# Optimization experiments

Hardware: AMD Instinct MI355X
Metric: run time of the kernel (lower is better)

## Reference

```python
import jax, jax.numpy as jnp
import numpy as np

N = 50000      # nodes
E = 800000     # edges (avg degree 16)
LM = 768       # lm_input_dim
H = 192        # hidden_dim = 32*6
B6 = 32        # per-branch dim = hidden_dim/6
SLOPE = 0.01   # nn.LeakyReLU default negative slope


def setup_inputs() -> dict:
    key = jax.random.key(0)
    ks = jax.random.split(key, 32)
    f = lambda i, shape, s=0.05: (jax.random.normal(ks[i], shape, jnp.float32) * s)
    inp = {
        "pre_x": f(0, (N, LM)),
        "x": f(1, (N, LM)),
        "edge_index": jax.random.randint(ks[2], (2, E), 0, N),
        "edge_type": jax.random.randint(ks[3], (E,), 0, 3),
        "num_prop": f(4, (N, 5)),
        "num_category": f(5, (N, 1)),
        "des_tensor": f(6, (N, LM)),
        "tweet_tensor": f(7, (N, LM)),
        # parameters (torch nn.Linear convention: W is [out, in], y = x @ W.T + b)
        "W_des": f(8, (B6, LM)), "b_des": f(9, (B6,)),
        "W_tweet": f(10, (B6, LM)), "b_tweet": f(11, (B6,)),
        "W_tweet_tr": f(12, (B6, LM)), "b_tweet_tr": f(13, (B6,)),
        "W_prop": f(14, (B6, 5)), "b_prop": f(15, (B6,)),
        "W_cat": f(16, (B6, 1)), "b_cat": f(17, (B6,)),
        "W_text": f(18, (B6, LM)), "b_text": f(19, (B6,)),
        "W_in": f(20, (H, H)), "b_in": f(21, (H,)),
        "W_c1": f(22, (H, H)), "b_c1": f(23, (H,)),
        "W_c2": f(24, (H, H)), "b_c2": f(25, (H,)),
        "W_o1": f(26, (96, H)), "b_o1": f(27, (96,)),
        "W_o2": f(28, (2, 96)), "b_o2": f(29, (2,)),
    }
    return inp


def _gcn_conv(h, W, b, src, dst):
    """PyG GCNConv: symmetric-normalized aggregation with added self-loops.
    out[v] = sum_{u->v} (d_u d_v)^{-1/2} (h_u W^T) + (1/d_v) (h_v W^T) + b
    where d includes the self-loop (+1)."""
    n = h.shape[0]
    hW = h @ W.T                                                  # [N, H]
    deg = jax.ops.segment_sum(jnp.ones(src.shape[0], h.dtype), dst,
                              num_segments=n) + 1.0               # [N]
    dinv = jax.lax.rsqrt(deg)
    norm = dinv[src] * dinv[dst]                                  # [E]
    agg = jax.ops.segment_sum(hW[src] * norm[:, None], dst,
                              num_segments=n)                     # [N, H]
    return agg + hW * (1.0 / deg)[:, None] + b


def reference(pre_x, x, edge_index, edge_type, num_prop, num_category,
              des_tensor, tweet_tensor,
              W_des, b_des, W_tweet, b_tweet, W_tweet_tr, b_tweet_tr,
              W_prop, b_prop, W_cat, b_cat, W_text, b_text,
              W_in, b_in, W_c1, b_c1, W_c2, b_c2,
              W_o1, b_o1, W_o2, b_o2):
    lrelu = lambda v: jax.nn.leaky_relu(v, SLOPE)
    branch = lambda t, W, b: lrelu(t @ W.T + b)   # dropout is identity in eval

    d = branch(des_tensor, W_des, b_des)
    pre_t = branch(pre_x, W_tweet, b_tweet)
    t = branch(x, W_tweet_tr, b_tweet_tr)
    n = branch(num_prop, W_prop, b_prop)
    c = branch(num_category, W_cat, b_cat)
    tw = branch(tweet_tensor, W_text, b_text)

    h = jnp.concatenate((n, c, d, tw, pre_t, t), axis=1)          # [N, 192]
    h = lrelu(h @ W_in.T + b_in)

    src, dst = edge_index[0], edge_index[1]
    h = _gcn_conv(h, W_c1, b_c1, src, dst)
    h = _gcn_conv(h, W_c2, b_c2, src, dst)

    em = lrelu(h @ W_o1.T + b_o1)                                 # [N, 96]
    out = em @ W_o2.T + b_o2                                      # [N, 2]
    return (out, em)
```

## Files before the change

kernel.cpp:

```cpp
#include <hip/hip_runtime.h>

#define NN 50000
#define EE 800000
#define LMD 768
#define HD 192
#define SLOPE 0.01f

typedef short bf16x8 __attribute__((ext_vector_type(8)));
typedef float f32x4 __attribute__((ext_vector_type(4)));
typedef unsigned short u16;

__device__ __forceinline__ float lrelu(float v){ return v > 0.f ? v : SLOPE * v; }

__device__ __forceinline__ u16 f2bf(float f){
    unsigned u = __float_as_uint(f);
    u += 0x7FFF + ((u >> 16) & 1u);
    return (u16)(u >> 16);
}
__device__ __forceinline__ float bf2f(u16 v){
    return __uint_as_float(((unsigned)v) << 16);
}
__device__ __forceinline__ bf16x8 as_bf8(float4 v){
    union { float4 f; bf16x8 b; } u; u.f = v; return u.b;
}

__global__ __launch_bounds__(256) void k_prep(
    const float* __restrict__ W0, const float* __restrict__ W1,
    const float* __restrict__ W2, const float* __restrict__ W3,
    const float* __restrict__ Win, const float* __restrict__ Wc1,
    const float* __restrict__ Wc2, const float* __restrict__ Wo1,
    u16* __restrict__ out)
{
    int m = blockIdx.y;
    int idx = blockIdx.x * 256 + threadIdx.x;
    const float* src; int nelem; int K;
    switch (m) {
      case 0: src = W0;  nelem = 32*768;  K = 768; break;
      case 1: src = W1;  nelem = 32*768;  K = 768; break;
      case 2: src = W2;  nelem = 32*768;  K = 768; break;
      case 3: src = W3;  nelem = 32*768;  K = 768; break;
      case 4: src = Win; nelem = 192*192; K = 192; break;
      case 5: src = Wc1; nelem = 192*192; K = 192; break;
      case 6: src = Wc2; nelem = 192*192; K = 192; break;
      default: src = Wo1; nelem = 96*192; K = 192; break;
    }
    if (idx >= nelem) return;
    u16 v = f2bf(src[idx]);
    int c = idx / K, k = idx - c * K;
    int cb = c >> 4, lr = c & 15;
    int sg = k >> 5, kk = k & 31, hi = kk >> 3, j = kk & 7;
    int lane = hi * 16 + lr;
    size_t dst;
    if (m < 4)      dst = (size_t)m * 24576 + (sg * 2 + cb) * 512 + lane * 8 + j;
    else if (m < 7) dst = 98304 + (size_t)(m - 4) * 36864 + (sg * 12 + cb) * 512 + lane * 8 + j;
    else            dst = 208896 + (size_t)(sg * 6 + cb) * 512 + lane * 8 + j;
    out[dst] = v;
}

#define BR_LOAD(R0, R1, c) { \
  _Pragma("unroll") for (int rt = 0; rt < 4; ++rt) { \
    const float* p_ = abase[rt] + (c) * 128; \
    R0[rt] = *(const float4*)p_; R1[rt] = *(const float4*)(p_ + 4); } \
  _Pragma("unroll") for (int rt = 0; rt < 4; ++rt) { \
    asm volatile("" :: "v"(R0[rt].x), "v"(R0[rt].y), "v"(R0[rt].z), "v"(R0[rt].w)); \
    asm volatile("" :: "v"(R1[rt].x), "v"(R1[rt].y), "v"(R1[rt].z), "v"(R1[rt].w)); } }

#define BR_WRITE(R0, R1) { \
  _Pragma("unroll") for (int rt = 0; rt < 4; ++rt) { \
    uint4 pk_; \
    pk_.x = (unsigned)f2bf(R0[rt].x) | ((unsigned)f2bf(R0[rt].y) << 16); \
    pk_.y = (unsigned)f2bf(R0[rt].z) | ((unsigned)f2bf(R0[rt].w) << 16); \
    pk_.z = (unsigned)f2bf(R1[rt].x) | ((unsigned)f2bf(R1[rt].y) << 16); \
    pk_.w = (unsigned)f2bf(R1[rt].z) | ((unsigned)f2bf(R1[rt].w) << 16); \
    *(uint4*)(Asg + wrIdx[rt]) = pk_; } }

#define BR_COMPUTE(fb) { \
  _Pragma("unroll") for (int sgl = 0; sgl < 4; ++sgl) { \
    bf16x8 af_ = *(const bf16x8*)(Asg + wbase + sgl * 512 + rdOff); \
    _Pragma("unroll") for (int cb = 0; cb < 2; ++cb) { \
      bf16x8 bf_ = *(const bf16x8*)(Bs + (fb) + (sgl * 2 + cb) * 512 + l * 8); \
      acc[cb] = __builtin_amdgcn_mfma_f32_16x16x32_bf16(af_, bf_, acc[cb], 0, 0, 0); } } }

#define BR_STAGEB(half) { \
  const uint4* s_ = (const uint4*)(Wb + (half) * 12288); uint4* d_ = (uint4*)Bs; \
  _Pragma("unroll") for (int i = 0; i < 6; ++i) d_[i * 256 + t] = s_[i * 256 + t]; }

__global__ __launch_bounds__(256) void k_branch(
    const float* __restrict__ des, const float* __restrict__ twt,
    const float* __restrict__ prex, const float* __restrict__ xx,
    const u16* __restrict__ Wf,
    const float* __restrict__ bd, const float* __restrict__ btx,
    const float* __restrict__ btw, const float* __restrict__ btr,
    u16* __restrict__ h)
{
    __shared__ u16 Bs[12288];
    __shared__ u16 Asg[8192];
    const int br = blockIdx.y;
    const float* A; const float* bias; int colBase;
    switch (br) {
      case 0:  A = des;  bias = bd;  colBase = 64;  break;
      case 1:  A = twt;  bias = btx; colBase = 96;  break;
      case 2:  A = prex; bias = btw; colBase = 128; break;
      default: A = xx;   bias = btr; colBase = 160; break;
    }
    const u16* Wb = Wf + br * 24576;

    const int t = threadIdx.x, w = t >> 6, l = t & 63;
    const int hi = l >> 4, lr = l & 15;
    const int rowBase = blockIdx.x * 64;
    const int wbase = w * 2048;
    const int rdOff = (l ^ hi) * 8;

    const float* abase[4];
    int wrIdx[4];
    #pragma unroll
    for (int rt = 0; rt < 4; ++rt) {
        int r = rowBase + w * 16 + rt * 4 + hi;
        if (r >= NN) r = NN - 1;
        abase[rt] = A + (size_t)r * LMD + lr * 8;
        int slot = ((l & 3) << 4) | (rt * 4 + hi);
        wrIdx[rt] = wbase + (lr >> 2) * 512 + (slot ^ (l & 3)) * 8;
    }

    f32x4 acc[2] = {};
    float4 a0[4], a1[4], b0[4], b1[4];

    BR_LOAD(a0, a1, 0);
    BR_STAGEB(0);
    __syncthreads();
    BR_LOAD(b0, b1, 1);
    BR_WRITE(a0, a1);  BR_COMPUTE(0);
    BR_LOAD(a0, a1, 2);
    BR_WRITE(b0, b1);  BR_COMPUTE(4096);
    BR_LOAD(b0, b1, 3);
    BR_WRITE(a0, a1);  BR_COMPUTE(8192);
    __syncthreads();
    BR_STAGEB(1);
    __syncthreads();
    BR_LOAD(a0, a1, 4);
    BR_WRITE(b0, b1);  BR_COMPUTE(0);
    BR_LOAD(b0, b1, 5);
    BR_WRITE(a0, a1);  BR_COMPUTE(4096);
    BR_WRITE(b0, b1);  BR_COMPUTE(8192);

    #pragma unroll
    for (int cb = 0; cb < 2; ++cb) {
        int cl = cb * 16 + lr;
        float bv = bias[cl];
        #pragma unroll
        for (int rg = 0; rg < 4; ++rg) {
            int r = rowBase + w * 16 + hi * 4 + rg;
            if (r < NN)
                h[(size_t)r * HD + colBase + cl] = f2bf(lrelu(acc[cb][rg] + bv));
        }
    }
}

template<bool BIAS, bool LRELU>
__global__ __launch_bounds__(512) void k_hgemm(
    const u16* __restrict__ A, const u16* __restrict__ Wf,
    const float* __restrict__ bias, u16* __restrict__ out)
{
    __shared__ u16 Bs[36864];
    const int t = threadIdx.x, w = t >> 6, l = t & 63;
    const int hi = l >> 4, lr = l & 15;
    const int rowBase = blockIdx.x * 128;
    {
        const uint4* s_ = (const uint4*)Wf; uint4* d_ = (uint4*)Bs;
        #pragma unroll
        for (int i = 0; i < 9; ++i) d_[i * 512 + t] = s_[i * 512 + t];
    }
    int r0 = rowBase + w * 16 + lr;
    int rowc = r0 < NN ? r0 : NN - 1;
    const u16* ap = A + (size_t)rowc * HD;
    float4 araw[6];
    #pragma unroll
    for (int sg = 0; sg < 6; ++sg) {
        araw[sg] = *(const float4*)(ap + sg * 32 + hi * 8);
        asm volatile("" :: "v"(araw[sg].x), "v"(araw[sg].y), "v"(araw[sg].z), "v"(araw[sg].w));
    }
    __syncthreads();

    f32x4 acc[12] = {};
    #pragma unroll
    for (int sg = 0; sg < 6; ++sg) {
        bf16x8 af = as_bf8(araw[sg]);
        #pragma unroll
        for (int cb = 0; cb < 12; ++cb) {
            bf16x8 bf = *(const bf16x8*)(Bs + (sg * 12 + cb) * 512 + l * 8);
            acc[cb] = __builtin_amdgcn_mfma_f32_16x16x32_bf16(af, bf, acc[cb], 0, 0, 0);
        }
    }

    #pragma unroll
    for (int cb = 0; cb < 12; ++cb) {
        int cl = cb * 16 + lr;
        float bv = BIAS ? bias[cl] : 0.f;
        #pragma unroll
        for (int rg = 0; rg < 4; ++rg) {
            int r = rowBase + w * 16 + hi * 4 + rg;
            if (r < NN) {
                float v = acc[cb][rg] + bv;
                if (LRELU) v = lrelu(v);
                out[(size_t)r * HD + cl] = f2bf(v);
            }
        }
    }
}

__global__ __launch_bounds__(512) void k_final(
    const u16* __restrict__ A, const u16* __restrict__ Wf,
    const float* __restrict__ b1, const float* __restrict__ W2,
    const float* __restrict__ b2, float* __restrict__ em, float* __restrict__ out)
{
    __shared__ u16 Bs[18432];
    const int t = threadIdx.x, w = t >> 6, l = t & 63;
    const int hi = l >> 4, lr = l & 15;
    const int rowBase = blockIdx.x * 128;
    {
        const uint4* s_ = (const uint4*)Wf; uint4* d_ = (uint4*)Bs;
        #pragma unroll
        for (int i = 0; i < 5; ++i) { int idx = i * 512 + t; if (idx < 2304) d_[idx] = s_[idx]; }
    }
    int r0 = rowBase + w * 16 + lr;
    int rowc = r0 < NN ? r0 : NN - 1;
    const u16* ap = A + (size_t)rowc * HD;
    float4 araw[6];
    #pragma unroll
    for (int sg = 0; sg < 6; ++sg) {
        araw[sg] = *(const float4*)(ap + sg * 32 + hi * 8);
        asm volatile("" :: "v"(araw[sg].x), "v"(araw[sg].y), "v"(araw[sg].z), "v"(araw[sg].w));
    }
    __syncthreads();

    f32x4 acc[6] = {};
    #pragma unroll
    for (int sg = 0; sg < 6; ++sg) {
        bf16x8 af = as_bf8(araw[sg]);
        #pragma unroll
        for (int cb = 0; cb < 6; ++cb) {
            bf16x8 bf = *(const bf16x8*)(Bs + (sg * 6 + cb) * 512 + l * 8);
            acc[cb] = __builtin_amdgcn_mfma_f32_16x16x32_bf16(af, bf, acc[cb], 0, 0, 0);
        }
    }

    float w2v[2][6], bv[6];
    #pragma unroll
    for (int cb = 0; cb < 6; ++cb) {
        bv[cb] = b1[cb * 16 + lr];
        w2v[0][cb] = W2[cb * 16 + lr];
        w2v[1][cb] = W2[96 + cb * 16 + lr];
    }

    #pragma unroll
    for (int rg = 0; rg < 4; ++rg) {
        int r = rowBase + w * 16 + hi * 4 + rg;
        float o0 = 0.f, o1 = 0.f;
        #pragma unroll
        for (int cb = 0; cb < 6; ++cb) {
            float v = lrelu(acc[cb][rg] + bv[cb]);
            if (r < NN) em[(size_t)r * 96 + cb * 16 + lr] = v;
            o0 += v * w2v[0][cb];
            o1 += v * w2v[1][cb];
        }
        #pragma unroll
        for (int d = 1; d < 16; d <<= 1) {
            o0 += __shfl_xor(o0, d);
            o1 += __shfl_xor(o1, d);
        }
        if (lr == 0 && r < NN) {
            out[r * 2 + 0] = o0 + b2[0];
            out[r * 2 + 1] = o1 + b2[1];
        }
    }
}

__global__ __launch_bounds__(256) void k_small_branch(
    const float* __restrict__ nprop, const float* __restrict__ ncat,
    const float* __restrict__ Wp, const float* __restrict__ bp,
    const float* __restrict__ Wc, const float* __restrict__ bc,
    u16* __restrict__ h)
{
    int idx = blockIdx.x * 256 + threadIdx.x;
    if (idx >= NN * 64) return;
    int row = idx >> 6, c = idx & 63;
    float acc;
    if (c < 32) {
        acc = bp[c];
        #pragma unroll
        for (int k = 0; k < 5; ++k) acc += nprop[row * 5 + k] * Wp[c * 5 + k];
    } else {
        int cc = c - 32;
        acc = bc[cc] + ncat[row] * Wc[cc];
    }
    h[(size_t)row * HD + c] = f2bf(lrelu(acc));
}

__global__ void k_count(const int* __restrict__ ei, int* __restrict__ deg)
{
    int e = blockIdx.x * 256 + threadIdx.x;
    if (e < EE) atomicAdd(&deg[ei[EE + e]], 1);
}

__global__ void k_deginv(const int* __restrict__ deg, float* __restrict__ dinv, float* __restrict__ invdeg)
{
    int v = blockIdx.x * 256 + threadIdx.x;
    if (v < NN) {
        float d = (float)(deg[v] + 1);
        dinv[v] = rsqrtf(d);
        invdeg[v] = 1.0f / d;
    }
}

__global__ __launch_bounds__(1024) void k_scan1(const int* __restrict__ deg, int* __restrict__ rp, int* __restrict__ part)
{
    __shared__ int sh[1024];
    int tid = threadIdx.x, i = blockIdx.x * 1024 + tid;
    int x = (i < NN) ? deg[i] : 0;
    sh[tid] = x;
    __syncthreads();
    for (int off = 1; off < 1024; off <<= 1) {
        int y = (tid >= off) ? sh[tid - off] : 0;
        __syncthreads();
        sh[tid] += y;
        __syncthreads();
    }
    if (i < NN) rp[i] = sh[tid] - x;
    if (tid == 1023) part[blockIdx.x] = sh[tid];
}

__global__ void k_scan2(int* part, int nb, int* rp)
{
    if (threadIdx.x == 0 && blockIdx.x == 0) {
        int run = 0;
        for (int b = 0; b < nb; ++b) { int t = part[b]; part[b] = run; run += t; }
        rp[NN] = run;
    }
}

__global__ void k_scan3(int* rp, const int* __restrict__ part)
{
    int i = blockIdx.x * 256 + threadIdx.x;
    if (i < NN) rp[i] += part[i >> 10];
}

__global__ void k_fill(const int* __restrict__ ei, const float* __restrict__ dinv,
                       int* __restrict__ cursor, int* __restrict__ cs, float* __restrict__ nrm)
{
    int e = blockIdx.x * 256 + threadIdx.x;
    if (e >= EE) return;
    int s = ei[e], d = ei[EE + e];
    int pos = atomicAdd(&cursor[d], 1);
    cs[pos] = s;
    nrm[pos] = dinv[s] * dinv[d];
}

__global__ __launch_bounds__(240) void k_agg(const u16* __restrict__ hW,
    const int* __restrict__ rp, const int* __restrict__ cs, const float* __restrict__ nrm,
    const float* __restrict__ invdeg, const float* __restrict__ bias, u16* __restrict__ out)
{
    int v = blockIdx.x * 5 + threadIdx.y;
    int f0 = threadIdx.x * 4;
    int s0 = rp[v], s1 = rp[v + 1];
    float4 bv = *reinterpret_cast<const float4*>(bias + f0);
    ushort4 hv = *reinterpret_cast<const ushort4*>(hW + (size_t)v * HD + f0);
    float idg = invdeg[v];
    float a0 = bf2f(hv.x) * idg + bv.x;
    float a1 = bf2f(hv.y) * idg + bv.y;
    float a2 = bf2f(hv.z) * idg + bv.z;
    float a3 = bf2f(hv.w) * idg + bv.w;
    int i = s0;
    for (; i + 4 <= s1; i += 4) {
        int c0 = cs[i], c1 = cs[i+1], c2 = cs[i+2], c3 = cs[i+3];
        float n0 = nrm[i], n1 = nrm[i+1], n2 = nrm[i+2], n3 = nrm[i+3];
        ushort4 g0 = *reinterpret_cast<const ushort4*>(hW + (size_t)c0 * HD + f0);
        ushort4 g1 = *reinterpret_cast<const ushort4*>(hW + (size_t)c1 * HD + f0);
        ushort4 g2 = *reinterpret_cast<const ushort4*>(hW + (size_t)c2 * HD + f0);
        ushort4 g3 = *reinterpret_cast<const ushort4*>(hW + (size_t)c3 * HD + f0);
        a0 += bf2f(g0.x) * n0; a1 += bf2f(g0.y) * n0; a2 += bf2f(g0.z) * n0; a3 += bf2f(g0.w) * n0;
        a0 += bf2f(g1.x) * n1; a1 += bf2f(g1.y) * n1; a2 += bf2f(g1.z) * n1; a3 += bf2f(g1.w) * n1;
        a0 += bf2f(g2.x) * n2; a1 += bf2f(g2.y) * n2; a2 += bf2f(g2.z) * n2; a3 += bf2f(g2.w) * n2;
        a0 += bf2f(g3.x) * n3; a1 += bf2f(g3.y) * n3; a2 += bf2f(g3.z) * n3; a3 += bf2f(g3.w) * n3;
    }
    for (; i < s1; ++i) {
        int c = cs[i]; float n = nrm[i];
        ushort4 g = *reinterpret_cast<const ushort4*>(hW + (size_t)c * HD + f0);
        a0 += bf2f(g.x) * n; a1 += bf2f(g.y) * n; a2 += bf2f(g.z) * n; a3 += bf2f(g.w) * n;
    }
    ushort4 o;
    o.x = f2bf(a0); o.y = f2bf(a1); o.z = f2bf(a2); o.w = f2bf(a3);
    *reinterpret_cast<ushort4*>(out + (size_t)v * HD + f0) = o;
}

extern "C" void kernel_launch(void* const* d_in, const int* in_sizes, int n_in,
                              void* d_out, int out_size, void* d_ws, size_t ws_size,
                              hipStream_t stream)
{
    const float* pre_x = (const float*)d_in[0];
    const float* x     = (const float*)d_in[1];
    const int*   ei    = (const int*)d_in[2];
    const float* nprop = (const float*)d_in[4];
    const float* ncat  = (const float*)d_in[5];
    const float* des   = (const float*)d_in[6];
    const float* twt   = (const float*)d_in[7];
    const float* W_des  = (const float*)d_in[8],  *b_des  = (const float*)d_in[9];
    const float* W_tw   = (const float*)d_in[10], *b_tw   = (const float*)d_in[11];
    const float* W_tr   = (const float*)d_in[12], *b_tr   = (const float*)d_in[13];
    const float* W_prop = (const float*)d_in[14], *b_prop = (const float*)d_in[15];
    const float* W_cat  = (const float*)d_in[16], *b_cat  = (const float*)d_in[17];
    const float* W_text = (const float*)d_in[18], *b_text = (const float*)d_in[19];
    const float* W_in   = (const float*)d_in[20], *b_in   = (const float*)d_in[21];
    const float* W_c1   = (const float*)d_in[22], *b_c1   = (const float*)d_in[23];
    const float* W_c2   = (const float*)d_in[24], *b_c2   = (const float*)d_in[25];
    const float* W_o1   = (const float*)d_in[26], *b_o1   = (const float*)d_in[27];
    const float* W_o2   = (const float*)d_in[28], *b_o2   = (const float*)d_in[29];

    char* base = (char*)d_ws;
    size_t off = 0;
    auto alloc = [&](size_t bytes) -> char* {
        char* p = base + off;
        off = (off + bytes + 255) & ~(size_t)255;
        return p;
    };
    u16*   hA     = (u16*)alloc((size_t)NN * HD * 2);
    u16*   hB     = (u16*)alloc((size_t)NN * HD * 2);
    u16*   hC     = (u16*)alloc((size_t)NN * HD * 2);
    u16*   Wprep  = (u16*)alloc((size_t)227328 * 2);
    float* dinv   = (float*)alloc((size_t)NN * 4);
    float* invdeg = (float*)alloc((size_t)NN * 4);
    int*   deg    = (int*)alloc((size_t)NN * 4);
    int*   rp     = (int*)alloc((size_t)(NN + 1) * 4);
    int*   cursor = (int*)alloc((size_t)NN * 4);
    int*   part   = (int*)alloc(64 * 4);
    int*   cs     = (int*)alloc((size_t)EE * 4);
    float* nrm    = (float*)alloc((size_t)EE * 4);
    (void)ws_size; (void)in_sizes; (void)n_in; (void)out_size;

    float* outp = (float*)d_out;
    float* em   = outp + (size_t)NN * 2;

    const int rb     = (NN + 255) / 256;
    const int rb64   = (NN + 63) / 64;
    const int rb128  = (NN + 127) / 128;
    const int eb     = (EE + 255) / 256;
    const int nb1024 = (NN + 1023) / 1024;

    hipMemsetAsync(deg, 0, (size_t)NN * 4, stream);
    hipLaunchKernelGGL(k_prep, dim3(144, 8), dim3(256), 0, stream,
        W_des, W_text, W_tw, W_tr, W_in, W_c1, W_c2, W_o1, Wprep);
    hipLaunchKernelGGL(k_count,  dim3(eb), dim3(256), 0, stream, ei, deg);
    hipLaunchKernelGGL(k_deginv, dim3(rb), dim3(256), 0, stream, deg, dinv, invdeg);
    hipLaunchKernelGGL(k_scan1,  dim3(nb1024), dim3(1024), 0, stream, deg, rp, part);
    hipLaunchKernelGGL(k_scan2,  dim3(1), dim3(1), 0, stream, part, nb1024, rp);
    hipLaunchKernelGGL(k_scan3,  dim3(rb), dim3(256), 0, stream, rp, part);
    hipMemcpyAsync(cursor, rp, (size_t)NN * 4, hipMemcpyDeviceToDevice, stream);
    hipLaunchKernelGGL(k_fill,   dim3(eb), dim3(256), 0, stream, ei, dinv, cursor, cs, nrm);

    hipLaunchKernelGGL(k_branch, dim3(rb64, 4), dim3(256), 0, stream,
        des, twt, pre_x, x, Wprep, b_des, b_text, b_tw, b_tr, hA);
    hipLaunchKernelGGL(k_small_branch, dim3((NN * 64 + 255) / 256), dim3(256), 0, stream,
        nprop, ncat, W_prop, b_prop, W_cat, b_cat, hA);

    hipLaunchKernelGGL((k_hgemm<true, true>),   dim3(rb128), dim3(512), 0, stream,
        hA, Wprep + 98304, b_in, hB);
    hipLaunchKernelGGL((k_hgemm<false, false>), dim3(rb128), dim3(512), 0, stream,
        hB, Wprep + 98304 + 36864, nullptr, hC);
    hipLaunchKernelGGL(k_agg, dim3(NN / 5), dim3(48, 5), 0, stream, hC, rp, cs, nrm, invdeg, b_c1, hA);
    hipLaunchKernelGGL((k_hgemm<false, false>), dim3(rb128), dim3(512), 0, stream,
        hA, Wprep + 98304 + 2 * 36864, nullptr, hB);
    hipLaunchKernelGGL(k_agg, dim3(NN / 5), dim3(48, 5), 0, stream, hB, rp, cs, nrm, invdeg, b_c2, hC);

    hipLaunchKernelGGL(k_final, dim3(rb128), dim3(512), 0, stream,
        hC, Wprep + 208896, b_o1, W_o2, b_o2, em, outp);
}
```

Before: 410.2 us.

## Stream branch activations via direct global-to-LDS loads with triple buffering

Rewrites the branch GEMM kernel to stage fp32 activation tiles straight into LDS using global_load_lds in a three-deep ring, with explicit vmcnt waits. The whole 32x768 weight slice now sits in LDS up front instead of being staged in two halves. This removes the register round-trip and the bf16 pack/write step for A, plus two block barriers. In exchange, bf16 conversion now happens after each LDS read, LDS use grows, and there are no barriers between waves (each wave reads only its own rows, which is fine).

```diff
diff --git a/kernel.cpp b/kernel.cpp
--- a/kernel.cpp
+++ b/kernel.cpp
@@ -23,6 +23,10 @@
 __device__ __forceinline__ bf16x8 as_bf8(float4 v){
     union { float4 f; bf16x8 b; } u; u.f = v; return u.b;
 }
+
+#define GLOAD16(gp, lp) __builtin_amdgcn_global_load_lds( \
+    (const __attribute__((address_space(1))) void*)(gp), \
+    (__attribute__((address_space(3))) void*)(lp), 16, 0, 0)
 
 __global__ __launch_bounds__(256) void k_prep(
     const float* __restrict__ W0, const float* __restrict__ W1,
@@ -57,34 +61,6 @@
     out[dst] = v;
 }
 
-#define BR_LOAD(R0, R1, c) { \
-  _Pragma("unroll") for (int rt = 0; rt < 4; ++rt) { \
-    const float* p_ = abase[rt] + (c) * 128; \
-    R0[rt] = *(const float4*)p_; R1[rt] = *(const float4*)(p_ + 4); } \
-  _Pragma("unroll") for (int rt = 0; rt < 4; ++rt) { \
-    asm volatile("" :: "v"(R0[rt].x), "v"(R0[rt].y), "v"(R0[rt].z), "v"(R0[rt].w)); \
-    asm volatile("" :: "v"(R1[rt].x), "v"(R1[rt].y), "v"(R1[rt].z), "v"(R1[rt].w)); } }
-
-#define BR_WRITE(R0, R1) { \
-  _Pragma("unroll") for (int rt = 0; rt < 4; ++rt) { \
-    uint4 pk_; \
-    pk_.x = (unsigned)f2bf(R0[rt].x) | ((unsigned)f2bf(R0[rt].y) << 16); \
-    pk_.y = (unsigned)f2bf(R0[rt].z) | ((unsigned)f2bf(R0[rt].w) << 16); \
-    pk_.z = (unsigned)f2bf(R1[rt].x) | ((unsigned)f2bf(R1[rt].y) << 16); \
-    pk_.w = (unsigned)f2bf(R1[rt].z) | ((unsigned)f2bf(R1[rt].w) << 16); \
-    *(uint4*)(Asg + wrIdx[rt]) = pk_; } }
-
-#define BR_COMPUTE(fb) { \
-  _Pragma("unroll") for (int sgl = 0; sgl < 4; ++sgl) { \
-    bf16x8 af_ = *(const bf16x8*)(Asg + wbase + sgl * 512 + rdOff); \
-    _Pragma("unroll") for (int cb = 0; cb < 2; ++cb) { \
-      bf16x8 bf_ = *(const bf16x8*)(Bs + (fb) + (sgl * 2 + cb) * 512 + l * 8); \
-      acc[cb] = __builtin_amdgcn_mfma_f32_16x16x32_bf16(af_, bf_, acc[cb], 0, 0, 0); } } }
-
-#define BR_STAGEB(half) { \
-  const uint4* s_ = (const uint4*)(Wb + (half) * 12288); uint4* d_ = (uint4*)Bs; \
-  _Pragma("unroll") for (int i = 0; i < 6; ++i) d_[i * 256 + t] = s_[i * 256 + t]; }
-
 __global__ __launch_bounds__(256) void k_branch(
     const float* __restrict__ des, const float* __restrict__ twt,
     const float* __restrict__ prex, const float* __restrict__ xx,
@@ -93,8 +69,9 @@
     const float* __restrict__ btw, const float* __restrict__ btr,
     u16* __restrict__ h)
 {
-    __shared__ u16 Bs[12288];
-    __shared__ u16 Asg[8192];
+    __shared__ u16 Ws_[24576];
+    __shared__ float Ab[3][64][32];
+
     const int br = blockIdx.y;
     const float* A; const float* bias; int colBase;
     switch (br) {
@@ -103,45 +80,60 @@
       case 2:  A = prex; bias = btw; colBase = 128; break;
       default: A = xx;   bias = btr; colBase = 160; break;
     }
-    const u16* Wb = Wf + br * 24576;
 
     const int t = threadIdx.x, w = t >> 6, l = t & 63;
     const int hi = l >> 4, lr = l & 15;
     const int rowBase = blockIdx.x * 64;
-    const int wbase = w * 2048;
-    const int rdOff = (l ^ hi) * 8;
-
-    const float* abase[4];
-    int wrIdx[4];
-    #pragma unroll
-    for (int rt = 0; rt < 4; ++rt) {
-        int r = rowBase + w * 16 + rt * 4 + hi;
-        if (r >= NN) r = NN - 1;
-        abase[rt] = A + (size_t)r * LMD + lr * 8;
-        int slot = ((l & 3) << 4) | (rt * 4 + hi);
-        wrIdx[rt] = wbase + (lr >> 2) * 512 + (slot ^ (l & 3)) * 8;
-    }
+
+    {
+        const uint4* s_ = (const uint4*)(Wf + br * 24576);
+        uint4* d_ = (uint4*)Ws_;
+        #pragma unroll
+        for (int i = 0; i < 12; ++i) d_[i * 256 + t] = s_[i * 256 + t];
+    }
+    __syncthreads();
+
+    const int rl_ = w * 16 + (l >> 3);
+    const int s16 = l & 7, g_ = s16 >> 1, hf = s16 & 1;
+
+#define STAGE(cc, bufi) { \
+    _Pragma("unroll") for (int i_ = 0; i_ < 2; ++i_) { \
+        int rl = rl_ + i_ * 8; \
+        int rg = rowBase + rl; if (rg >= NN) rg = NN - 1; \
+        const float* gp = A + (size_t)rg * LMD + (cc) * 32 + ((g_ ^ (rl & 3)) * 8 + hf * 4); \
+        GLOAD16(gp, &Ab[bufi][w * 16 + i_ * 8][0]); } }
+
+    STAGE(0, 0);
+    STAGE(1, 1);
 
     f32x4 acc[2] = {};
-    float4 a0[4], a1[4], b0[4], b1[4];
-
-    BR_LOAD(a0, a1, 0);
-    BR_STAGEB(0);
-    __syncthreads();
-    BR_LOAD(b0, b1, 1);
-    BR_WRITE(a0, a1);  BR_COMPUTE(0);
-    BR_LOAD(a0, a1, 2);
-    BR_WRITE(b0, b1);  BR_COMPUTE(4096);
-    BR_LOAD(b0, b1, 3);
-    BR_WRITE(a0, a1);  BR_COMPUTE(8192);
-    __syncthreads();
-    BR_STAGEB(1);
-    __syncthreads();
-    BR_LOAD(a0, a1, 4);
-    BR_WRITE(b0, b1);  BR_COMPUTE(0);
-    BR_LOAD(b0, b1, 5);
-    BR_WRITE(a0, a1);  BR_COMPUTE(4096);
-    BR_WRITE(b0, b1);  BR_COMPUTE(8192);
+
+    #pragma unroll
+    for (int c = 0; c < 24; ++c) {
+        if (c + 2 < 24) {
+            const int bufi = (c + 2) % 3;
+            STAGE(c + 2, bufi);
+        }
+        if (c < 22)      { asm volatile("s_waitcnt vmcnt(4)" ::: "memory"); }
+        else if (c == 22){ asm volatile("s_waitcnt vmcnt(2)" ::: "memory"); }
+        else             { asm volatile("s_waitcnt vmcnt(0)" ::: "memory"); }
+        __builtin_amdgcn_sched_barrier(0);
+
+        const float* ab = &Ab[c % 3][w * 16 + lr][(hi ^ (lr & 3)) * 8];
+        float4 lo = *(const float4*)ab;
+        float4 hp = *(const float4*)(ab + 4);
+        bf16x8 af;
+        af[0] = (short)f2bf(lo.x); af[1] = (short)f2bf(lo.y);
+        af[2] = (short)f2bf(lo.z); af[3] = (short)f2bf(lo.w);
+        af[4] = (short)f2bf(hp.x); af[5] = (short)f2bf(hp.y);
+        af[6] = (short)f2bf(hp.z); af[7] = (short)f2bf(hp.w);
+        #pragma unroll
+        for (int cb = 0; cb < 2; ++cb) {
+            bf16x8 bf = *(const bf16x8*)(Ws_ + (c * 2 + cb) * 512 + l * 8);
+            acc[cb] = __builtin_amdgcn_mfma_f32_16x16x32_bf16(af, bf, acc[cb], 0, 0, 0);
+        }
+    }
+#undef STAGE
 
     #pragma unroll
     for (int cb = 0; cb < 2; ++cb) {
```

Result: no change. 405.3 us (-1.2%).
